# Performance work log

Measured on AMD Instinct MI355X. Metric: run time of the kernel, lower is better.

The kernel has to match this reference:

```python
import jax, jax.numpy as jnp
import numpy as np

B, S, D = 2, 2048, 2048
H, DH = 16, 128          # n_heads, head_dim
HFF = 8192               # hidden_dim (SwiGLU)
EPS = 1e-5               # layer_norm_eps passed to AdvancedRMSNorm


def setup_inputs() -> dict:
    key = jax.random.key(0)
    ks = jax.random.split(key, 16)
    sd = lambda fan_in: 1.0 / np.sqrt(fan_in)
    inp = {
        "x": jax.random.normal(ks[0], (B, S, D), jnp.float32),
        # attention (torch Linear weights: [out, in])
        "q_w": jax.random.normal(ks[1], (D, D), jnp.float32) * sd(D),
        "k_w": jax.random.normal(ks[2], (D, D), jnp.float32) * sd(D),
        "v_w": jax.random.normal(ks[3], (D, D), jnp.float32) * sd(D),
        "o_w": jax.random.normal(ks[4], (D, D), jnp.float32) * sd(D),
        "temp": jnp.ones((H, 1, 1), jnp.float32),  # learnable per-head temperature
        # RMSNorm scales
        "ln1_w": jnp.ones((D,), jnp.float32),
        "ln2_w": jnp.ones((D,), jnp.float32),
        # SwiGLU
        "gate_w": jax.random.normal(ks[5], (HFF, D), jnp.float32) * sd(D),
        "up_w": jax.random.normal(ks[6], (HFF, D), jnp.float32) * sd(D),
        "gate2_w": jax.random.normal(ks[7], (HFF, D), jnp.float32) * sd(D),
        "down_w": jax.random.normal(ks[8], (D, HFF), jnp.float32) * sd(HFF),
        # gated residual connections (Linear with bias)
        "ag_w": jax.random.normal(ks[9], (D, D), jnp.float32) * sd(D),
        "ag_b": jnp.zeros((D,), jnp.float32),
        "fg_w": jax.random.normal(ks[10], (D, D), jnp.float32) * sd(D),
        "fg_b": jnp.zeros((D,), jnp.float32),
    }
    return inp


def _rmsnorm(x, w):
    rms = jnp.sqrt(jnp.mean(x * x, axis=-1, keepdims=True) + EPS)
    return w * (x / rms)


def _l2norm(x):
    # F.normalize(dim=-1): x / max(||x||_2, 1e-12)
    n = jnp.sqrt(jnp.sum(x * x, axis=-1, keepdims=True))
    return x / jnp.maximum(n, 1e-12)


def _block(x, q_w, k_w, v_w, o_w, temp, ln1_w, ln2_w,
           gate_w, up_w, gate2_w, down_w, ag_w, ag_b, fg_w, fg_b):
    # --- cosine-sim attention sublayer ---
    residual = x
    h = _rmsnorm(x, ln1_w)
    q = (h @ q_w.T).reshape(B, S, H, DH).transpose(0, 2, 1, 3)  # [B,H,S,DH]
    k = (h @ k_w.T).reshape(B, S, H, DH).transpose(0, 2, 1, 3)
    v = (h @ v_w.T).reshape(B, S, H, DH).transpose(0, 2, 1, 3)
    q = _l2norm(q)
    k = _l2norm(k)
    scores = jnp.einsum("bhqd,bhkd->bhqk", q, k) * temp  # temp [H,1,1] broadcasts
    causal = jnp.triu(jnp.ones((S, S), bool), k=1)
    scores = jnp.where(causal, -jnp.inf, scores)
    attn = jax.nn.softmax(scores, axis=-1)
    out = jnp.einsum("bhqk,bhkd->bhqd", attn, v)
    out = out.transpose(0, 2, 1, 3).reshape(B, S, D)
    attn_out = out @ o_w.T
    # gated residual: sigmoid(W a + b)*a + (1-g)*residual
    g = jax.nn.sigmoid(attn_out @ ag_w.T + ag_b)
    x = g * attn_out + (1.0 - g) * residual
    # --- SwiGLU sublayer ---
    residual = x
    h = _rmsnorm(x, ln2_w)
    gate = jax.nn.silu(h @ gate_w.T)
    up = h @ up_w.T
    gate2 = jax.nn.sigmoid(h @ gate2_w.T)
    ffn_out = (gate * up * gate2) @ down_w.T
    g = jax.nn.sigmoid(ffn_out @ fg_w.T + fg_b)
    return g * ffn_out + (1.0 - g) * residual


def reference(x, q_w, k_w, v_w, o_w, temp, ln1_w, ln2_w,
              gate_w, up_w, gate2_w, down_w, ag_w, ag_b, fg_w, fg_b):
    return _block(x, q_w, k_w, v_w, o_w, temp, ln1_w, ln2_w,
                  gate_w, up_w, gate2_w, down_w, ag_w, ag_b, fg_w, fg_b)
```

## Files before the change

### kernel.cpp

```cpp
#include <hip/hip_runtime.h>

typedef unsigned short u16;
typedef unsigned int u32;
using bf16x8 = __attribute__((ext_vector_type(8))) short;
using f32x4  = __attribute__((ext_vector_type(4))) float;

#define EPS 1e-5f

__device__ __forceinline__ u16 f2bf(float f) {
    union { float f; u32 u; } v; v.f = f;
    u32 r = v.u + 0x7FFFu + ((v.u >> 16) & 1u);
    return (u16)(r >> 16);
}
__device__ __forceinline__ float bf2f(u16 u) {
    union { u32 u; float f; } v; v.u = ((u32)u) << 16;
    return v.f;
}
__device__ __forceinline__ u32 pack2(float a, float b) {
    return (u32)f2bf(a) | ((u32)f2bf(b) << 16);
}
__device__ __forceinline__ void gl16(const void* g, void* s) {
    __builtin_amdgcn_global_load_lds(
        (const __attribute__((address_space(1))) u32*)g,
        (__attribute__((address_space(3))) u32*)s, 16, 0, 0);
}
__device__ __forceinline__ float sigm(float x) { return 1.f / (1.f + __expf(-x)); }

__global__ void conv_bf16(const float* __restrict__ src, u16* __restrict__ dst, int n4) {
    int i = blockIdx.x * 256 + threadIdx.x;
    if (i >= n4) return;
    float4 v = reinterpret_cast<const float4*>(src)[i];
    u32 lo = (u32)f2bf(v.x) | ((u32)f2bf(v.y) << 16);
    u32 hi = (u32)f2bf(v.z) | ((u32)f2bf(v.w) << 16);
    reinterpret_cast<uint2*>(dst)[i] = make_uint2(lo, hi);
}

__global__ void conv3_bf16(const float* __restrict__ s0, const float* __restrict__ s1,
                           const float* __restrict__ s2, u16* __restrict__ d0,
                           u16* __restrict__ d1, u16* __restrict__ d2, int n4) {
    int i = blockIdx.x * 256 + threadIdx.x;
    if (i >= n4) return;
    const float* src = (blockIdx.y == 0) ? s0 : (blockIdx.y == 1) ? s1 : s2;
    u16* dst = (blockIdx.y == 0) ? d0 : (blockIdx.y == 1) ? d1 : d2;
    float4 v = reinterpret_cast<const float4*>(src)[i];
    u32 lo = (u32)f2bf(v.x) | ((u32)f2bf(v.y) << 16);
    u32 hi = (u32)f2bf(v.z) | ((u32)f2bf(v.w) << 16);
    reinterpret_cast<uint2*>(dst)[i] = make_uint2(lo, hi);
}

__global__ void rmsnorm_k(const float* __restrict__ x, const float* __restrict__ wt,
                          u16* __restrict__ out) {
    __shared__ float red[4];
    const int row = blockIdx.x, t = threadIdx.x;
    const float* xr = x + (size_t)row * 2048;
    float4 v0 = *reinterpret_cast<const float4*>(&xr[t * 8]);
    float4 v1 = *reinterpret_cast<const float4*>(&xr[t * 8 + 4]);
    float ss = v0.x*v0.x + v0.y*v0.y + v0.z*v0.z + v0.w*v0.w
             + v1.x*v1.x + v1.y*v1.y + v1.z*v1.z + v1.w*v1.w;
#pragma unroll
    for (int d = 1; d < 64; d <<= 1) ss += __shfl_xor(ss, d);
    if ((t & 63) == 0) red[t >> 6] = ss;
    __syncthreads();
    const float tot = red[0] + red[1] + red[2] + red[3];
    const float s = 1.f / sqrtf(tot * (1.f / 2048.f) + EPS);
    float4 w0 = *reinterpret_cast<const float4*>(&wt[t * 8]);
    float4 w1 = *reinterpret_cast<const float4*>(&wt[t * 8 + 4]);
    u32 o[4];
    o[0] = pack2(v0.x * s * w0.x, v0.y * s * w0.y);
    o[1] = pack2(v0.z * s * w0.z, v0.w * s * w0.w);
    o[2] = pack2(v1.x * s * w1.x, v1.y * s * w1.y);
    o[3] = pack2(v1.z * s * w1.z, v1.w * s * w1.w);
    *reinterpret_cast<uint4*>(&out[(size_t)row * 2048 + t * 8]) =
        make_uint4(o[0], o[1], o[2], o[3]);
}

__global__ void qk_l2norm(u16* __restrict__ qkv, const float* __restrict__ temp) {
    const int wid = blockIdx.x * 4 + (threadIdx.x >> 6);
    const int l = threadIdx.x & 63;
    const int n = wid >> 5;
    const int rem = wid & 31;
    const int which = rem >> 4;
    const int h = rem & 15;
    u16* p = qkv + (size_t)n * 6144 + which * 2048 + h * 128 + l * 2;
    u32 v = *reinterpret_cast<const u32*>(p);
    float f0 = bf2f((u16)(v & 0xffff)), f1 = bf2f((u16)(v >> 16));
    float ss = f0 * f0 + f1 * f1;
#pragma unroll
    for (int d = 1; d < 64; d <<= 1) ss += __shfl_xor(ss, d);
    float sc = 1.f / fmaxf(sqrtf(ss), 1e-12f);
    if (which == 0) sc *= temp[h];
    *reinterpret_cast<u32*>(p) = pack2(f0 * sc, f1 * sc);
}

__global__ __launch_bounds__(512, 1)
void gemm_swiglu(const u16* __restrict__ A, const u16* __restrict__ W0,
                 const u16* __restrict__ W1, u16* __restrict__ combo, int K) {
    extern __shared__ u16 lds[];
    const int orig = blockIdx.x;
    const int xcd = orig & 7, lin = orig >> 3;
    const int wgid = xcd * 32 + lin;
    const int qsel = wgid & 1;
    const int tix = wgid >> 1;
    const int g = tix >> 5;
    const int rem = tix & 31;
    const int bn = rem >> 2;
    const int bm = (g << 2) + (rem & 3);
    const u16* B = qsel ? W1 : W0;

    const int t = threadIdx.x;
    const int w = t >> 6, l = t & 63;
    const int wr = w >> 2, wc = w & 3;
    const int lr = l & 15, lg = l >> 4;
    const int NT = K >> 6;

    const int srow = t >> 3;
    const int scg  = (t & 7) ^ (srow & 7);
    const u16* aS0 = A + (size_t)(bm * 256 + srow) * K + scg * 8;
    const u16* aS1 = aS0 + (size_t)128 * K;
    const size_t r64 = (size_t)64 * K;

#define STG(slot, src, ko) do {                                     \
        gl16((src) + (ko), (slot) + t * 8);                         \
        gl16((src) + (ko) + r64, (slot) + 4096 + t * 8);            \
    } while (0)

    const int xr = (lr & 7) << 4;
    const int kof[2] = { ((lg) << 4) ^ xr, ((4 + lg) << 4) ^ xr };

    f32x4 acc[8][4];
    u32 pk[8][4][2];

    for (int pan = 0; pan < 3; ++pan) {
        const u16* bS0 = B + (size_t)(pan * 2048 + bn * 256 + srow) * K + scg * 8;
        const u16* bS1 = bS0 + (size_t)128 * K;
        {
            u16* bb = lds;
            STG(bb + 16384, bS0, 0);
            STG(bb + 24576, bS1, 0);
            STG(bb + 0,     aS0, 0);
            STG(bb + 8192,  aS1, 0);
        }
        if (pan == 1) {
#pragma unroll
            for (int m = 0; m < 8; m++)
#pragma unroll
                for (int n = 0; n < 4; n++)
#pragma unroll
                    for (int h = 0; h < 2; h++) {
                        const float a0 = acc[m][n][2 * h], a1 = acc[m][n][2 * h + 1];
                        pk[m][n][h] = pack2(a0 * sigm(a0), a1 * sigm(a1));
                    }
        } else if (pan == 2) {
#pragma unroll
            for (int m = 0; m < 8; m++)
#pragma unroll
                for (int n = 0; n < 4; n++)
#pragma unroll
                    for (int h = 0; h < 2; h++) {
                        const u32 sv = pk[m][n][h];
                        const float t0 = bf2f((u16)(sv & 0xffff)) * acc[m][n][2 * h];
                        const float t1 = bf2f((u16)(sv >> 16)) * acc[m][n][2 * h + 1];
                        pk[m][n][h] = pack2(t0, t1);
                    }
        }
        asm volatile("s_waitcnt vmcnt(0)" ::: "memory");
        __builtin_amdgcn_s_barrier();

#pragma unroll
        for (int i = 0; i < 8; i++)
#pragma unroll
            for (int j = 0; j < 4; j++) acc[i][j] = (f32x4){0.f, 0.f, 0.f, 0.f};

        for (int T = 0; T < NT; ++T) {
            const char* base = (const char*)lds + (size_t)(T & 1) * 65536;
            u16* sb = lds + ((T + 1) & 1) * 32768;
            const bool st = (T + 1) < NT;
            const size_t ko = (size_t)(T + 1) * 64;
            const char* aB = base + wr * 16384;
            const char* bB = base + 32768 + (wc >> 1) * 16384 + (wc & 1) * 8192;
            bf16x8 bfr[4][2];
#pragma unroll
            for (int n = 0; n < 4; n++) {
                const int rb = n * 16 + lr;
                bfr[n][0] = *reinterpret_cast<const bf16x8*>(bB + rb * 128 + kof[0]);
                bfr[n][1] = *reinterpret_cast<const bf16x8*>(bB + rb * 128 + kof[1]);
            }
#pragma unroll
            for (int p = 0; p < 4; ++p) {
                const int ks = p >> 1, mh = p & 1;
                bf16x8 af[4];
#pragma unroll
                for (int m2 = 0; m2 < 4; m2++) {
                    const int ra = mh * 64 + m2 * 16 + lr;
                    af[m2] = *reinterpret_cast<const bf16x8*>(aB + ra * 128 + kof[ks]);
                }
                if (st) {
                    if (p == 0) STG(sb + 16384, bS0, ko);
                    if (p == 1) STG(sb + 24576, bS1, ko);
                    if (p == 2) STG(sb + 0,     aS0, ko);
                    if (p == 3) STG(sb + 8192,  aS1, ko);
                }
                __builtin_amdgcn_s_setprio(1);
#pragma unroll
                for (int m2 = 0; m2 < 4; m2++)
#pragma unroll
                    for (int n = 0; n < 4; n++)
                        acc[mh * 4 + m2][n] = __builtin_amdgcn_mfma_f32_16x16x32_bf16(
                            af[m2], bfr[n][ks], acc[mh * 4 + m2][n], 0, 0, 0);
                __builtin_amdgcn_s_setprio(0);
            }
            if (st) {
                asm volatile("s_waitcnt vmcnt(0)" ::: "memory");
                __builtin_amdgcn_s_barrier();
            }
        }
    }
#undef STG

    const int cbase = qsel * 2048 + bn * 256;
#pragma unroll
    for (int m = 0; m < 8; m++) {
        const int row = bm * 256 + wr * 128 + m * 16 + lg * 4;
#pragma unroll
        for (int n = 0; n < 4; n++) {
            const int col = cbase + wc * 64 + n * 16 + lr;
#pragma unroll
            for (int h = 0; h < 2; h++) {
                const u32 tv = pk[m][n][h];
                const float o0 = bf2f((u16)(tv & 0xffff)) * sigm(acc[m][n][2 * h]);
                const float o1 = bf2f((u16)(tv >> 16)) * sigm(acc[m][n][2 * h + 1]);
                combo[(size_t)(row + 2 * h) * 8192 + col] = f2bf(o0);
                combo[(size_t)(row + 2 * h + 1) * 8192 + col] = f2bf(o1);
            }
        }
    }
}

template <int EPI>
__global__ __launch_bounds__(512, 1)
void gemm_u(const u16* __restrict__ A, const u16* __restrict__ B,
            float* __restrict__ outF, u16* __restrict__ outB,
            const float* __restrict__ bias, const float* __restrict__ addend,
            const float* __restrict__ resid, float* __restrict__ outG,
            int M, int N, int K, int ldc) {
    extern __shared__ u16 lds[];
    const int nbn = N >> 8;
    const int nwg = (M >> 7) * nbn;
    const int orig = blockIdx.x;
    const int q8 = nwg >> 3, r8 = nwg & 7;
    const int xcd = orig & 7, lin = orig >> 3;
    const int wgid = (xcd < r8 ? xcd * (q8 + 1) : r8 * (q8 + 1) + (xcd - r8) * q8) + lin;
    const int g = wgid / (nbn << 3);
    const int rem = wgid - g * (nbn << 3);
    const int bn = rem >> 3;
    const int bm = (g << 3) + (rem & 7);

    const int t = threadIdx.x;
    const int w = t >> 6, l = t & 63;
    const int wr = w >> 2, wc = w & 3;
    const int lr = l & 15, lg = l >> 4;
    const int NT = K >> 6;

    const int pr = t >> 3, ps = t & 7;
    const int sg = ps ^ (pr & 7);
    const u16* aSrc = A + (size_t)(bm * 128 + pr) * K + sg * 8;
    const u16* bSrc = B + (size_t)(bn * 256 + pr) * K + sg * 8;
    const size_t rowStep = (size_t)64 * K;

#define STG_A(bi, ko) do { u16* da = lds + (bi) * 24576 + t * 8;                 \
        gl16(aSrc + (ko), da); gl16(aSrc + rowStep + (ko), da + 4096); } while (0)
#define STG_B01(bi, ko) do { u16* db = lds + (bi) * 24576 + 8192 + t * 8;        \
        gl16(bSrc + (ko), db); gl16(bSrc + rowStep + (ko), db + 4096); } while (0)
#define STG_B23(bi, ko) do { u16* db = lds + (bi) * 24576 + 8192 + t * 8;        \
        gl16(bSrc + 2 * rowStep + (ko), db + 8192);                              \
        gl16(bSrc + 3 * rowStep + (ko), db + 12288); } while (0)

    f32x4 acc[4][4];
#pragma unroll
    for (int i = 0; i < 4; i++)
#pragma unroll
        for (int j = 0; j < 4; j++) acc[i][j] = (f32x4){0.f, 0.f, 0.f, 0.f};

    const int xr = (lr & 7) << 4;
    const int kof[2] = { ((lg) << 4) ^ xr, ((4 + lg) << 4) ^ xr };

    STG_A(0, 0); STG_B01(0, 0); STG_B23(0, 0);
    asm volatile("s_waitcnt vmcnt(0)" ::: "memory");
    __builtin_amdgcn_s_barrier();

    for (int T = 0; T < NT; ++T) {
        const char* bufA = (const char*)lds + (size_t)(T & 1) * 49152;
        const char* bufB = bufA + 16384;
        const int sbi = (T + 1) & 1;
        const bool st = (T + 1) < NT;
        const size_t ko = (size_t)(T + 1) * 64;
        bf16x8 bf[4][2];
#pragma unroll
        for (int n = 0; n < 4; n++) {
            const int rb = wc * 64 + n * 16 + lr;
            bf[n][0] = *reinterpret_cast<const bf16x8*>(bufB + rb * 128 + kof[0]);
            bf[n][1] = *reinterpret_cast<const bf16x8*>(bufB + rb * 128 + kof[1]);
        }
#pragma unroll
        for (int p = 0; p < 4; ++p) {
            const int ks = p >> 1, mh = p & 1;
            bf16x8 af[2];
#pragma unroll
            for (int m2 = 0; m2 < 2; m2++) {
                const int ra = wr * 64 + (mh * 2 + m2) * 16 + lr;
                af[m2] = *reinterpret_cast<const bf16x8*>(bufA + ra * 128 + kof[ks]);
            }
            if (st) {
                if (p == 0) STG_A(sbi, ko);
                if (p == 1) STG_B01(sbi, ko);
                if (p == 2) STG_B23(sbi, ko);
            }
            __builtin_amdgcn_s_setprio(1);
#pragma unroll
            for (int m2 = 0; m2 < 2; m2++)
#pragma unroll
                for (int n = 0; n < 4; n++)
                    acc[mh * 2 + m2][n] = __builtin_amdgcn_mfma_f32_16x16x32_bf16(
                        af[m2], bf[n][ks], acc[mh * 2 + m2][n], 0, 0, 0);
            __builtin_amdgcn_s_setprio(0);
        }
        if (st) {
            asm volatile("s_waitcnt vmcnt(0)" ::: "memory");
            __builtin_amdgcn_s_barrier();
        }
    }
#undef STG_A
#undef STG_B01
#undef STG_B23

#pragma unroll
    for (int m = 0; m < 4; m++) {
        const int row = bm * 128 + wr * 64 + m * 16 + lg * 4;
#pragma unroll
        for (int n = 0; n < 4; n++) {
            const int col = bn * 256 + wc * 64 + n * 16 + lr;
#pragma unroll
            for (int q = 0; q < 4; q++) {
                const size_t idx = (size_t)(row + q) * ldc + col;
                const float v = acc[m][n][q];
                if (EPI == 0) {
                    outB[idx] = f2bf(v);
                } else if (EPI == 1) {
                    outF[idx] = v;
                    outB[idx] = f2bf(v);
                } else {
                    const float g2 = sigm(v + bias[col]);
                    outG[idx] = g2 * addend[idx] + (1.f - g2) * resid[idx];
                }
            }
        }
    }
}

#define VSWZ(dh) (((((dh) >> 3) ^ (dh)) & 7) << 4)
__global__ __launch_bounds__(512) void flash_attn(const u16* __restrict__ qkv,
                                                  u16* __restrict__ out) {
    __shared__ u16 klds[2][64 * 128];
    __shared__ u16 vlds[2][128 * 64];
    __shared__ u16 plds[8][16 * 64];
    const int t = threadIdx.x, w = t >> 6, l = t & 63;
    const int lr = l & 15, lg = l >> 4;
    const int b0 = blockIdx.x;
    const int xcd = b0 & 7, i0 = b0 >> 3;
    const int bh = ((i0 & 3) << 3) | xcd;
    const int p = i0 >> 2;
    const int b = bh >> 4, h = bh & 15;
    const size_t base = (size_t)b * 2048;
    const int sr0 = t >> 4;
    const int sc0 = (t & 15) << 3;

    uint4 kreg0, kreg1, vreg0, vreg1;

#define STAGE_LOAD(KT) do {                                                          \
        const size_t gg = (base + (size_t)(KT) * 64 + sr0) * 6144 + h * 128 + sc0;   \
        kreg0 = *reinterpret_cast<const uint4*>(&qkv[gg + 2048]);                    \
        vreg0 = *reinterpret_cast<const uint4*>(&qkv[gg + 4096]);                    \
        kreg1 = *reinterpret_cast<const uint4*>(&qkv[gg + 32 * 6144 + 2048]);        \
        vreg1 = *reinterpret_cast<const uint4*>(&qkv[gg + 32 * 6144 + 4096]);        \
    } while (0)

#define STAGE_WRITE(BUF) do {                                                                     \
        char* kb = (char*)&klds[BUF][0];                                                          \
        char* vb = (char*)&vlds[BUF][0];                                                          \
        *reinterpret_cast<uint4*>(kb + ((sr0 * 256 + sc0 * 2) ^ ((sr0 & 7) << 4))) = kreg0;       \
        *reinterpret_cast<uint4*>(kb + (((sr0 + 32) * 256 + sc0 * 2) ^ ((sr0 & 7) << 4))) = kreg1;\
        union { uint4 u; u16 s[8]; } vv;                                                          \
        vv.u = vreg0;                                                                             \
        _Pragma("unroll")                                                                         \
        for (int jj = 0; jj < 8; jj++) {                                                          \
            const int dh = sc0 + jj;                                                              \
            *reinterpret_cast<u16*>(vb + ((dh * 128 + sr0 * 2) ^ VSWZ(dh))) = vv.s[jj];           \
        }                                                                                         \
        vv.u = vreg1;                                                                             \
        _Pragma("unroll")                                                                         \
        for (int jj = 0; jj < 8; jj++) {                                                          \
            const int dh = sc0 + jj;                                                              \
            *reinterpret_cast<u16*>(vb + ((dh * 128 + (sr0 + 32) * 2) ^ VSWZ(dh))) = vv.s[jj];    \
        }                                                                                         \
    } while (0)

    for (int phase = 0; phase < 2; ++phase) {
        const int qt = phase ? (15 - p) : p;
        const int last = 2 * qt + 1;
        const int qrow = qt * 128 + w * 16 + lr;
        const int qr0 = qt * 128 + w * 16 + lg * 4;
        bf16x8 qf[4];
#pragma unroll
        for (int kk = 0; kk < 4; kk++)
            qf[kk] = *reinterpret_cast<const bf16x8*>(
                &qkv[(base + qrow) * 6144 + h * 128 + kk * 32 + lg * 8]);
        f32x4 o[8];
#pragma unroll
        for (int i = 0; i < 8; i++) o[i] = (f32x4){0.f, 0.f, 0.f, 0.f};
        float m[4] = {-1e30f, -1e30f, -1e30f, -1e30f};
        float ls[4] = {0.f, 0.f, 0.f, 0.f};

        STAGE_LOAD(0);
        int cur = 0;
        STAGE_WRITE(0);
        __syncthreads();

        for (int kt = 0; kt <= last; ++kt) {
            if (kt < last) STAGE_LOAD(kt + 1);
            const char* kb = (const char*)&klds[cur][0];
            const char* vb = (const char*)&vlds[cur][0];
            f32x4 s[4];
#pragma unroll
            for (int nf = 0; nf < 4; nf++) {
                f32x4 a = (f32x4){0.f, 0.f, 0.f, 0.f};
                const int kv = nf * 16 + lr;
#pragma unroll
                for (int kk = 0; kk < 4; kk++) {
                    bf16x8 kf = *reinterpret_cast<const bf16x8*>(
                        kb + ((kv * 256 + kk * 64 + lg * 16) ^ ((kv & 7) << 4)));
                    a = __builtin_amdgcn_mfma_f32_16x16x32_bf16(qf[kk], kf, a, 0, 0, 0);
                }
                s[nf] = a;
            }
            if (kt >= 2 * qt) {
#pragma unroll
                for (int nf = 0; nf < 4; nf++) {
                    const int kvi = kt * 64 + nf * 16 + lr;
#pragma unroll
                    for (int q = 0; q < 4; q++)
                        if (kvi > qr0 + q) s[nf][q] = -1e30f;
                }
            }
            float mx[4] = {-1e30f, -1e30f, -1e30f, -1e30f};
#pragma unroll
            for (int nf = 0; nf < 4; nf++)
#pragma unroll
                for (int q = 0; q < 4; q++) mx[q] = fmaxf(mx[q], s[nf][q]);
#pragma unroll
            for (int q = 0; q < 4; q++) {
#pragma unroll
                for (int d = 1; d < 16; d <<= 1) mx[q] = fmaxf(mx[q], __shfl_xor(mx[q], d));
            }
            float fac[4], rs[4];
#pragma unroll
            for (int q = 0; q < 4; q++) {
                const float mn = fmaxf(m[q], mx[q]);
                fac[q] = __expf(m[q] - mn);
                m[q] = mn;
                rs[q] = 0.f;
            }
#pragma unroll
            for (int nf = 0; nf < 4; nf++) {
#pragma unroll
                for (int q = 0; q < 4; q++) {
                    const float pv = __expf(s[nf][q] - m[q]);
                    s[nf][q] = pv;
                    rs[q] += pv;
                }
            }
#pragma unroll
            for (int nf = 0; nf < 4; nf++) {
                const int col = nf * 16 + lr;
#pragma unroll
                for (int q = 0; q < 4; q++) {
                    const int row = lg * 4 + q;
                    *reinterpret_cast<u16*>((char*)&plds[w][0] +
                        ((row * 128 + col * 2) ^ ((row & 7) << 4))) = f2bf(s[nf][q]);
                }
            }
#pragma unroll
            for (int q = 0; q < 4; q++) {
#pragma unroll
                for (int d = 1; d < 16; d <<= 1) rs[q] += __shfl_xor(rs[q], d);
                ls[q] = ls[q] * fac[q] + rs[q];
            }
#pragma unroll
            for (int nf2 = 0; nf2 < 8; nf2++)
#pragma unroll
                for (int q = 0; q < 4; q++) o[nf2][q] *= fac[q];
#pragma unroll
            for (int ks = 0; ks < 2; ks++) {
                bf16x8 pf = *reinterpret_cast<const bf16x8*>((char*)&plds[w][0] +
                    ((lr * 128 + ks * 64 + lg * 16) ^ ((lr & 7) << 4)));
#pragma unroll
                for (int nf2 = 0; nf2 < 8; nf2++) {
                    const int dh = nf2 * 16 + lr;
                    bf16x8 vf = *reinterpret_cast<const bf16x8*>(
                        vb + ((dh * 128 + ks * 64 + lg * 16) ^ VSWZ(dh)));
                    o[nf2] = __builtin_amdgcn_mfma_f32_16x16x32_bf16(pf, vf, o[nf2], 0, 0, 0);
                }
            }
            if (kt < last) STAGE_WRITE(cur ^ 1);
            __syncthreads();
            cur ^= 1;
        }
#pragma unroll
        for (int nf2 = 0; nf2 < 8; nf2++) {
            const int col = h * 128 + nf2 * 16 + lr;
#pragma unroll
            for (int q = 0; q < 4; q++) {
                const float v = o[nf2][q] / ls[q];
                out[(base + qr0 + q) * 2048 + col] = f2bf(v);
            }
        }
        __syncthreads();
    }
#undef STAGE_LOAD
#undef STAGE_WRITE
}

extern "C" void kernel_launch(void* const* d_in, const int* in_sizes, int n_in,
                              void* d_out, int out_size, void* d_ws, size_t ws_size,
                              hipStream_t stream) {
    const float* x      = (const float*)d_in[0];
    const float* q_w    = (const float*)d_in[1];
    const float* k_w    = (const float*)d_in[2];
    const float* v_w    = (const float*)d_in[3];
    const float* o_w    = (const float*)d_in[4];
    const float* temp   = (const float*)d_in[5];
    const float* ln1_w  = (const float*)d_in[6];
    const float* ln2_w  = (const float*)d_in[7];
    const float* gate_w = (const float*)d_in[8];
    const float* up_w   = (const float*)d_in[9];
    const float* gate2_w= (const float*)d_in[10];
    const float* down_w = (const float*)d_in[11];
    const float* ag_w   = (const float*)d_in[12];
    const float* ag_b   = (const float*)d_in[13];
    const float* fg_w   = (const float*)d_in[14];
    const float* fg_b   = (const float*)d_in[15];

    const int GEMM_LDS = 98304;
    const int SW_LDS   = 131072;
    (void)hipFuncSetAttribute(reinterpret_cast<const void*>(&gemm_u<0>),
                              hipFuncAttributeMaxDynamicSharedMemorySize, GEMM_LDS);
    (void)hipFuncSetAttribute(reinterpret_cast<const void*>(&gemm_u<1>),
                              hipFuncAttributeMaxDynamicSharedMemorySize, GEMM_LDS);
    (void)hipFuncSetAttribute(reinterpret_cast<const void*>(&gemm_u<2>),
                              hipFuncAttributeMaxDynamicSharedMemorySize, GEMM_LDS);
    (void)hipFuncSetAttribute(reinterpret_cast<const void*>(&gemm_swiglu),
                              hipFuncAttributeMaxDynamicSharedMemorySize, SW_LDS);

    char* ws = (char*)d_ws;
    u16*  Wbuf = (u16*)(ws);
    u16*  hbuf = (u16*)(ws + 33554432);
    float* x1  = (float*)(ws + 50331648);
    u16*  combo= (u16*)(ws + 83886080);
    char* E    = ws + 150994944;
    char* F    = ws + 201326592;
    u16*  ffb  = (u16*)(ws + 234881024);

    u16*   qkvact = (u16*)E;
    float* aof    = (float*)E;
    u16*   aob    = (u16*)(E + 33554432);
    u16*   Wffn2  = (u16*)E;
    u16*   attnb  = (u16*)F;
    float* fff    = (float*)F;

    float* outp = (float*)d_out;
    const size_t DD = 2048ull * 2048ull;
    const int cg_d = (int)(DD / 4) / 256;
    const int GRID_BIG = 32 * 24;
    const int GRID_SM  = 32 * 8;

    hipLaunchKernelGGL(rmsnorm_k, dim3(4096), dim3(256), 0, stream, x, ln1_w, hbuf);

    hipLaunchKernelGGL(conv3_bf16, dim3(cg_d, 3), dim3(256), 0, stream,
                       q_w, k_w, v_w, Wbuf, Wbuf + DD, Wbuf + 2 * DD, (int)(DD / 4));
    hipLaunchKernelGGL((gemm_u<0>), dim3(GRID_BIG), dim3(512), GEMM_LDS, stream,
                       hbuf, Wbuf, (float*)nullptr, qkvact,
                       (const float*)nullptr, (const float*)nullptr, (const float*)nullptr,
                       (float*)nullptr, 4096, 6144, 2048, 6144);

    hipLaunchKernelGGL(qk_l2norm, dim3(32768), dim3(256), 0, stream, qkvact, temp);

    hipLaunchKernelGGL(flash_attn, dim3(256), dim3(512), 0, stream, qkvact, attnb);

    hipLaunchKernelGGL(conv_bf16, dim3(cg_d), dim3(256), 0, stream, o_w, Wbuf, (int)(DD / 4));
    hipLaunchKernelGGL((gemm_u<1>), dim3(GRID_SM), dim3(512), GEMM_LDS, stream,
                       attnb, Wbuf, aof, aob,
                       (const float*)nullptr, (const float*)nullptr, (const float*)nullptr,
                       (float*)nullptr, 4096, 2048, 2048, 2048);

    hipLaunchKernelGGL(conv_bf16, dim3(cg_d), dim3(256), 0, stream, ag_w, Wbuf, (int)(DD / 4));
    hipLaunchKernelGGL((gemm_u<2>), dim3(GRID_SM), dim3(512), GEMM_LDS, stream,
                       aob, Wbuf, (float*)nullptr, (u16*)nullptr,
                       ag_b, aof, x, x1, 4096, 2048, 2048, 2048);

    hipLaunchKernelGGL(rmsnorm_k, dim3(4096), dim3(256), 0, stream, x1, ln2_w, hbuf);

    for (int d = 0; d < 2; d++) {
        const size_t w0 = (size_t)(2 * d) * 2048 * 2048;
        const size_t w1 = (size_t)(2 * d + 1) * 2048 * 2048;
        hipLaunchKernelGGL(conv3_bf16, dim3(cg_d, 3), dim3(256), 0, stream,
                           gate_w + w0, up_w + w0, gate2_w + w0,
                           Wbuf, Wbuf + 2048 * 2048, Wbuf + 2ull * 2048 * 2048, (int)(DD / 4));
        hipLaunchKernelGGL(conv3_bf16, dim3(cg_d, 3), dim3(256), 0, stream,
                           gate_w + w1, up_w + w1, gate2_w + w1,
                           Wffn2, Wffn2 + 2048 * 2048, Wffn2 + 2ull * 2048 * 2048, (int)(DD / 4));
        hipLaunchKernelGGL(gemm_swiglu, dim3(256), dim3(512), SW_LDS, stream,
                           hbuf, Wbuf, Wffn2, combo + (size_t)d * 2 * 2048, 2048);
    }

    hipLaunchKernelGGL(conv_bf16, dim3(16384), dim3(256), 0, stream, down_w, Wbuf, (int)(2048ull * 8192 / 4));
    hipLaunchKernelGGL((gemm_u<1>), dim3(GRID_SM), dim3(512), GEMM_LDS, stream,
                       combo, Wbuf, fff, ffb,
                       (const float*)nullptr, (const float*)nullptr, (const float*)nullptr,
                       (float*)nullptr, 4096, 2048, 8192, 2048);

    hipLaunchKernelGGL(conv_bf16, dim3(cg_d), dim3(256), 0, stream, fg_w, Wbuf, (int)(DD / 4));
    hipLaunchKernelGGL((gemm_u<2>), dim3(GRID_SM), dim3(512), GEMM_LDS, stream,
                       ffb, Wbuf, (float*)nullptr, (u16*)nullptr,
                       fg_b, fff, x1, outp, 4096, 2048, 2048, 2048);
}
```

Measured before the change: 1.045 ms.

## Add dedicated 256x384-tile QKV GEMM and batch output-side weight conversions

Replaces the generic templated GEMM for the fused QKV projection with a dedicated kernel. It uses 256x384 output tiles, a double-buffered 160KB LDS pipeline and 8x6 MFMA accumulators per wave, so the whole 4096x6144 output fits in a single 256-block wave instead of several waves of smaller tiles. It also converts o_w, ag_w and fg_w to bf16 in one launch right after the QKV GEMM. Those weights are stored in separate workspace slots, and down_w moves to another region so the FFN loop does not overwrite them. The new kernel writes its output with scalar bf16 stores and needs much more LDS per block, so occupancy is limited to one block per CU.

```diff
diff --git a/kernel.cpp b/kernel.cpp
--- a/kernel.cpp
+++ b/kernel.cpp
@@ -90,6 +90,113 @@
     float sc = 1.f / fmaxf(sqrtf(ss), 1e-12f);
     if (which == 0) sc *= temp[h];
     *reinterpret_cast<u32*>(p) = pack2(f0 * sc, f1 * sc);
+}
+
+__global__ __launch_bounds__(512, 1)
+void gemm_qkv(const u16* __restrict__ A, const u16* __restrict__ B,
+              u16* __restrict__ outB, int K, int ldc) {
+    extern __shared__ u16 lds[];
+    const int orig = blockIdx.x;
+    const int xcd = orig & 7, lin = orig >> 3;
+    const int wgid = xcd * 32 + lin;
+    const int bm = wgid >> 4;
+    const int bn = wgid & 15;
+
+    const int t = threadIdx.x;
+    const int w = t >> 6, l = t & 63;
+    const int wr = w >> 2, wc = w & 3;
+    const int lr = l & 15, lg = l >> 4;
+    const int NT = K >> 6;
+
+    const int srow = t >> 3;
+    const int scg  = (t & 7) ^ (srow & 7);
+    const u16* aS0 = A + (size_t)(bm * 256 + srow) * K + scg * 8;
+    const u16* aS1 = aS0 + (size_t)128 * K;
+    const u16* bS0 = B + (size_t)(bn * 384 + srow) * K + scg * 8;
+    const u16* bS1 = bS0 + (size_t)128 * K;
+    const u16* bS2 = bS0 + (size_t)256 * K;
+    const size_t r64 = (size_t)64 * K;
+
+#define STG(slot, src, ko) do {                                     \
+        gl16((src) + (ko), (slot) + t * 8);                         \
+        gl16((src) + (ko) + r64, (slot) + 4096 + t * 8);            \
+    } while (0)
+#define STG_TILE(bi, ko) do {                                       \
+        u16* bb = lds + (size_t)(bi) * 40960;                       \
+        STG(bb + 0,     aS0, ko);                                   \
+        STG(bb + 8192,  aS1, ko);                                   \
+        STG(bb + 16384, bS0, ko);                                   \
+        STG(bb + 24576, bS1, ko);                                   \
+        STG(bb + 32768, bS2, ko);                                   \
+    } while (0)
+
+    f32x4 acc[8][6];
+#pragma unroll
+    for (int i = 0; i < 8; i++)
+#pragma unroll
+        for (int j = 0; j < 6; j++) acc[i][j] = (f32x4){0.f, 0.f, 0.f, 0.f};
+
+    const int xr = (lr & 7) << 4;
+    const int kof[2] = { ((lg) << 4) ^ xr, ((4 + lg) << 4) ^ xr };
+
+    STG_TILE(0, 0);
+    asm volatile("s_waitcnt vmcnt(0)" ::: "memory");
+    __builtin_amdgcn_s_barrier();
+
+    for (int T = 0; T < NT; ++T) {
+        const char* base = (const char*)lds + (size_t)(T & 1) * 81920;
+        u16* sb = lds + (size_t)((T + 1) & 1) * 40960;
+        const bool st = (T + 1) < NT;
+        const size_t ko = (size_t)(T + 1) * 64;
+        const char* aB = base + wr * 16384;
+        const char* bB = base + 32768 + wc * 12288;
+#pragma unroll
+        for (int ks = 0; ks < 2; ++ks) {
+            bf16x8 bfr[6];
+#pragma unroll
+            for (int n = 0; n < 6; n++)
+                bfr[n] = *reinterpret_cast<const bf16x8*>(bB + (n * 16 + lr) * 128 + kof[ks]);
+#pragma unroll
+            for (int mh = 0; mh < 2; ++mh) {
+                bf16x8 af[4];
+#pragma unroll
+                for (int m2 = 0; m2 < 4; m2++)
+                    af[m2] = *reinterpret_cast<const bf16x8*>(
+                        aB + (mh * 64 + m2 * 16 + lr) * 128 + kof[ks]);
+                if (st) {
+                    if (ks == 0 && mh == 0) { STG(sb + 0, aS0, ko); STG(sb + 8192, aS1, ko); }
+                    if (ks == 0 && mh == 1) { STG(sb + 16384, bS0, ko); STG(sb + 24576, bS1, ko); }
+                    if (ks == 1 && mh == 0) { STG(sb + 32768, bS2, ko); }
+                }
+                __builtin_amdgcn_s_setprio(1);
+#pragma unroll
+                for (int m2 = 0; m2 < 4; m2++)
+#pragma unroll
+                    for (int n = 0; n < 6; n++)
+                        acc[mh * 4 + m2][n] = __builtin_amdgcn_mfma_f32_16x16x32_bf16(
+                            af[m2], bfr[n], acc[mh * 4 + m2][n], 0, 0, 0);
+                __builtin_amdgcn_s_setprio(0);
+            }
+        }
+        if (st) {
+            asm volatile("s_waitcnt vmcnt(0)" ::: "memory");
+            __builtin_amdgcn_s_barrier();
+        }
+    }
+#undef STG
+#undef STG_TILE
+
+#pragma unroll
+    for (int m = 0; m < 8; m++) {
+        const int row = bm * 256 + wr * 128 + m * 16 + lg * 4;
+#pragma unroll
+        for (int n = 0; n < 6; n++) {
+            const int col = bn * 384 + wc * 96 + n * 16 + lr;
+#pragma unroll
+            for (int q = 0; q < 4; q++)
+                outB[(size_t)(row + q) * ldc + col] = f2bf(acc[m][n][q]);
+        }
+    }
 }
 
 __global__ __launch_bounds__(512, 1)
@@ -551,14 +658,15 @@
 
     const int GEMM_LDS = 98304;
     const int SW_LDS   = 131072;
-    (void)hipFuncSetAttribute(reinterpret_cast<const void*>(&gemm_u<0>),
-                              hipFuncAttributeMaxDynamicSharedMemorySize, GEMM_LDS);
+    const int QKV_LDS  = 163840;
     (void)hipFuncSetAttribute(reinterpret_cast<const void*>(&gemm_u<1>),
                               hipFuncAttributeMaxDynamicSharedMemorySize, GEMM_LDS);
     (void)hipFuncSetAttribute(reinterpret_cast<const void*>(&gemm_u<2>),
                               hipFuncAttributeMaxDynamicSharedMemorySize, GEMM_LDS);
     (void)hipFuncSetAttribute(reinterpret_cast<const void*>(&gemm_swiglu),
                               hipFuncAttributeMaxDynamicSharedMemorySize, SW_LDS);
+    (void)hipFuncSetAttribute(reinterpret_cast<const void*>(&gemm_qkv),
+                              hipFuncAttributeMaxDynamicSharedMemorySize, QKV_LDS);
 
     char* ws = (char*)d_ws;
     u16*  Wbuf = (u16*)(ws);
@@ -573,37 +681,36 @@
     float* aof    = (float*)E;
     u16*   aob    = (u16*)(E + 33554432);
     u16*   Wffn2  = (u16*)E;
+    u16*   Wdn    = (u16*)E;
     u16*   attnb  = (u16*)F;
     float* fff    = (float*)F;
 
     float* outp = (float*)d_out;
     const size_t DD = 2048ull * 2048ull;
     const int cg_d = (int)(DD / 4) / 256;
-    const int GRID_BIG = 32 * 24;
     const int GRID_SM  = 32 * 8;
 
     hipLaunchKernelGGL(rmsnorm_k, dim3(4096), dim3(256), 0, stream, x, ln1_w, hbuf);
 
     hipLaunchKernelGGL(conv3_bf16, dim3(cg_d, 3), dim3(256), 0, stream,
                        q_w, k_w, v_w, Wbuf, Wbuf + DD, Wbuf + 2 * DD, (int)(DD / 4));
-    hipLaunchKernelGGL((gemm_u<0>), dim3(GRID_BIG), dim3(512), GEMM_LDS, stream,
-                       hbuf, Wbuf, (float*)nullptr, qkvact,
-                       (const float*)nullptr, (const float*)nullptr, (const float*)nullptr,
-                       (float*)nullptr, 4096, 6144, 2048, 6144);
+    hipLaunchKernelGGL(gemm_qkv, dim3(256), dim3(512), QKV_LDS, stream,
+                       hbuf, Wbuf, qkvact, 2048, 6144);
+
+    hipLaunchKernelGGL(conv3_bf16, dim3(cg_d, 3), dim3(256), 0, stream,
+                       o_w, ag_w, fg_w, Wbuf, Wbuf + DD, Wbuf + 3 * DD, (int)(DD / 4));
 
     hipLaunchKernelGGL(qk_l2norm, dim3(32768), dim3(256), 0, stream, qkvact, temp);
 
     hipLaunchKernelGGL(flash_attn, dim3(256), dim3(512), 0, stream, qkvact, attnb);
 
-    hipLaunchKernelGGL(conv_bf16, dim3(cg_d), dim3(256), 0, stream, o_w, Wbuf, (int)(DD / 4));
     hipLaunchKernelGGL((gemm_u<1>), dim3(GRID_SM), dim3(512), GEMM_LDS, stream,
                        attnb, Wbuf, aof, aob,
                        (const float*)nullptr, (const float*)nullptr, (const float*)nullptr,
                        (float*)nullptr, 4096, 2048, 2048, 2048);
 
-    hipLaunchKernelGGL(conv_bf16, dim3(cg_d), dim3(256), 0, stream, ag_w, Wbuf, (int)(DD / 4));
     hipLaunchKernelGGL((gemm_u<2>), dim3(GRID_SM), dim3(512), GEMM_LDS, stream,
-                       aob, Wbuf, (float*)nullptr, (u16*)nullptr,
+                       aob, Wbuf + DD, (float*)nullptr, (u16*)nullptr,
                        ag_b, aof, x, x1, 4096, 2048, 2048, 2048);
 
     hipLaunchKernelGGL(rmsnorm_k, dim3(4096), dim3(256), 0, stream, x1, ln2_w, hbuf);
@@ -613,22 +720,21 @@
         const size_t w1 = (size_t)(2 * d + 1) * 2048 * 2048;
         hipLaunchKernelGGL(conv3_bf16, dim3(cg_d, 3), dim3(256), 0, stream,
                            gate_w + w0, up_w + w0, gate2_w + w0,
-                           Wbuf, Wbuf + 2048 * 2048, Wbuf + 2ull * 2048 * 2048, (int)(DD / 4));
+                           Wbuf, Wbuf + DD, Wbuf + 2 * DD, (int)(DD / 4));
         hipLaunchKernelGGL(conv3_bf16, dim3(cg_d, 3), dim3(256), 0, stream,
                            gate_w + w1, up_w + w1, gate2_w + w1,
-                           Wffn2, Wffn2 + 2048 * 2048, Wffn2 + 2ull * 2048 * 2048, (int)(DD / 4));
+                           Wffn2, Wffn2 + DD, Wffn2 + 2 * DD, (int)(DD / 4));
         hipLaunchKernelGGL(gemm_swiglu, dim3(256), dim3(512), SW_LDS, stream,
                            hbuf, Wbuf, Wffn2, combo + (size_t)d * 2 * 2048, 2048);
     }
 
-    hipLaunchKernelGGL(conv_bf16, dim3(16384), dim3(256), 0, stream, down_w, Wbuf, (int)(2048ull * 8192 / 4));
+    hipLaunchKernelGGL(conv_bf16, dim3(16384), dim3(256), 0, stream, down_w, Wdn, (int)(2048ull * 8192 / 4));
     hipLaunchKernelGGL((gemm_u<1>), dim3(GRID_SM), dim3(512), GEMM_LDS, stream,
-                       combo, Wbuf, fff, ffb,
+                       combo, Wdn, fff, ffb,
                        (const float*)nullptr, (const float*)nullptr, (const float*)nullptr,
                        (float*)nullptr, 4096, 2048, 8192, 2048);
 
-    hipLaunchKernelGGL(conv_bf16, dim3(cg_d), dim3(256), 0, stream, fg_w, Wbuf, (int)(DD / 4));
     hipLaunchKernelGGL((gemm_u<2>), dim3(GRID_SM), dim3(512), GEMM_LDS, stream,
-                       ffb, Wbuf, (float*)nullptr, (u16*)nullptr,
+                       ffb, Wbuf + 3 * DD, (float*)nullptr, (u16*)nullptr,
                        fg_b, fff, x1, outp, 4096, 2048, 2048, 2048);
 }
```

Measured after the change: 1.091 ms. 1.04x slower.
